# Performance work log

Measured on AMD Instinct MI355X. Metric: run time of the kernel, lower is better.

Reference implementation:

```python
import jax, jax.numpy as jnp
import numpy as np

K = 60
BATCH, NCLS, H, W = 8, 2, 512, 512


def _neighbors(x):
    # x: [B,H,W] int32 in {0,1}. Returns P2..P9 clockwise starting north.
    p = jnp.pad(x, ((0, 0), (1, 1), (1, 1)))
    P2 = p[:, :-2, 1:-1]   # N
    P3 = p[:, :-2, 2:]     # NE
    P4 = p[:, 1:-1, 2:]    # E
    P5 = p[:, 2:, 2:]      # SE
    P6 = p[:, 2:, 1:-1]    # S
    P7 = p[:, 2:, :-2]     # SW
    P8 = p[:, 1:-1, :-2]   # W
    P9 = p[:, :-2, :-2]    # NW
    return P2, P3, P4, P5, P6, P7, P8, P9


def _substep(x, first):
    # One Zhang-Suen thinning sub-iteration (the algorithm used by
    # skimage.morphology.skeletonize for 2D images).
    P2, P3, P4, P5, P6, P7, P8, P9 = _neighbors(x)
    seq = (P2, P3, P4, P5, P6, P7, P8, P9, P2)
    # A = number of 0->1 transitions in circular neighbor sequence
    A = sum(((seq[i] == 0) & (seq[i + 1] == 1)).astype(jnp.int32) for i in range(8))
    Bn = P2 + P3 + P4 + P5 + P6 + P7 + P8 + P9
    if first:
        c3 = P2 * P4 * P6
        c4 = P4 * P6 * P8
    else:
        c3 = P2 * P4 * P8
        c4 = P2 * P6 * P8
    delete = (x == 1) & (Bn >= 2) & (Bn <= 6) & (A == 1) & (c3 == 0) & (c4 == 0)
    return x * (1 - delete.astype(x.dtype))


def _skeletonize(img):
    # img: [B,H,W] int32 binary. Iterate thinning until fixed point.
    def body(state):
        x, _ = state
        x2 = _substep(_substep(x, True), False)
        return x2, jnp.any(x2 != x)

    def cond(state):
        return state[1]

    out, _ = jax.lax.while_loop(cond, body, (img, jnp.array(True)))
    return out


def _conv(x, kernel, pad):
    # x: [B,1,H,W], kernel: [1,1,k,k], 'same' padding pad
    return jax.lax.conv_general_dilated(x, kernel, (1, 1), [(pad, pad), (pad, pad)])


def setup_inputs() -> dict:
    key = jax.random.key(0)
    k1, k2 = jax.random.split(key)
    pred = jax.random.normal(k1, (BATCH, NCLS, H, W), dtype=jnp.float32)
    target = jax.random.randint(k2, (BATCH, H, W), 0, NCLS, dtype=jnp.int32)
    return {"pred": pred, "target": target}


def reference(pred, target):
    # Per-pixel cross entropy, reduction='none'
    logp = jax.nn.log_softmax(pred, axis=1)
    L = -jnp.take_along_axis(logp, target[:, None].astype(jnp.int32), axis=1)[:, 0]  # [B,H,W]

    # Skeletonize the hard prediction (nonzero = foreground)
    A = jnp.argmax(pred, axis=1)
    skel = _skeletonize((A != 0).astype(jnp.int32))  # [B,H,W]
    Bm = skel[:, None].astype(pred.dtype)            # [B,1,H,W]

    # 3x3 neighbor count (center zeroed); endpoints C where product == 1
    k3 = jnp.ones((1, 1, 3, 3), pred.dtype).at[0, 0, 1, 1].set(0.0)
    C = Bm * _conv(Bm, k3, 1)
    C = (C == 1.0).astype(pred.dtype)

    # 9x9 endpoint density, scaled by K; zeros -> weight 1
    k9 = jnp.ones((1, 1, 9, 9), pred.dtype)
    N = _conv(C, k9, 4) * K
    Wmap = N + (N == 0.0).astype(pred.dtype)  # [B,1,H,W]

    return jnp.mean(Wmap[:, 0] * L)
```

## Files before the change

### kernel.cpp

```cpp
#include <hip/hip_runtime.h>

#define BATCH   8
#define HH      512
#define WW      512
#define IMGPIX  (HH * WW)
#define NPIX    (BATCH * IMGPIX)
#define NWORDS  (NPIX / 64)
#define WPR     8
#define LDSTR   9
#define FPSCALE 262144.0
#define MAXPAIR 256

typedef unsigned long long u64;
typedef unsigned int u32;

__global__ void prep_kernel(const float* __restrict__ pred, const int* __restrict__ target,
                            float* __restrict__ L, u64* __restrict__ xp,
                            u64* __restrict__ acc64, u32* __restrict__ ticket) {
    int i = blockIdx.x * blockDim.x + threadIdx.x;
    if (i == 0) { acc64[0] = 0ULL; ticket[0] = 0u; }
    if (i >= NPIX) return;
    int b = i >> 18;
    int hw = i & (IMGPIX - 1);
    float p0 = pred[((size_t)(2 * b) << 18) + hw];
    float p1 = pred[((size_t)(2 * b + 1) << 18) + hw];
    float m = fmaxf(p0, p1);
    float lse = m + logf(expf(p0 - m) + expf(p1 - m));
    int t = target[i];
    L[i] = lse - (t ? p1 : p0);
    u64 word = __ballot(p1 > p0);
    if ((threadIdx.x & 63) == 0) xp[i >> 6] = word;
}

#define FA(a,b,c,s,cy) { u64 _x = (a)^(b); (s) = _x^(c); (cy) = ((a)&(b)) | ((c)&_x); }
#define HA(a,b,s,cy)   { (s) = (a)^(b); (cy) = (a)&(b); }

template<int FIRST>
__device__ __forceinline__ u64 zs_row(const u64* __restrict__ U, u64* __restrict__ M,
                                      const u64* __restrict__ D)
{
    u64 ch = 0;
    #pragma unroll
    for (int k = 0; k < WPR; ++k) {
        u64 Mc = M[k];
        if (Mc == 0ULL) continue;
        u64 Uc = U[k], Dc = D[k];
        u64 Up = k     ? U[k-1] : 0ULL;
        u64 Mp = k     ? M[k-1] : 0ULL;
        u64 Dp = k     ? D[k-1] : 0ULL;
        u64 Un = k < 7 ? U[k+1] : 0ULL;
        u64 Mn = k < 7 ? M[k+1] : 0ULL;
        u64 Dn = k < 7 ? D[k+1] : 0ULL;
        u64 P2 = Uc, P6 = Dc;
        u64 P3 = (Uc >> 1) | (Un << 63);
        u64 P4 = (Mc >> 1) | (Mn << 63);
        u64 P5 = (Dc >> 1) | (Dn << 63);
        u64 P9 = (Uc << 1) | (Up >> 63);
        u64 P8 = (Mc << 1) | (Mp >> 63);
        u64 P7 = (Dc << 1) | (Dp >> 63);

        u64 sa,ca, sb,cb, sc,cc, b0,cd, sd,ce, b1,cf, b2,b3;
        FA(P2,P3,P4, sa,ca);
        FA(P5,P6,P7, sb,cb);
        FA(P8,P9,sa, sc,cc);
        HA(sb,sc,    b0,cd);
        FA(ca,cb,cc, sd,ce);
        HA(sd,cd,    b1,cf);
        HA(ce,cf,    b2,b3);
        u64 ge2 = b1 | b2 | b3;
        u64 le6 = ~(b3 | (b0 & b1 & b2));

        u64 e, seen, two = 0;
        seen = (~P2) & P3;
        e = (~P3) & P4; two |= seen & e; seen |= e;
        e = (~P4) & P5; two |= seen & e; seen |= e;
        e = (~P5) & P6; two |= seen & e; seen |= e;
        e = (~P6) & P7; two |= seen & e; seen |= e;
        e = (~P7) & P8; two |= seen & e; seen |= e;
        e = (~P8) & P9; two |= seen & e; seen |= e;
        e = (~P9) & P2; two |= seen & e; seen |= e;
        u64 A1 = seen & ~two;

        u64 c34;
        if (FIRST) { u64 t = P4 & P6; c34 = t & (P2 | P8); }
        else       { u64 t = P2 & P8; c34 = t & (P4 | P6); }

        u64 del = Mc & ge2 & le6 & A1 & ~c34;
        M[k] = Mc ^ del;
        ch |= del;
    }
    return ch;
}

__global__ __launch_bounds__(512)
void skel_kernel(const u64* __restrict__ xp, u64* __restrict__ eg)
{
    __shared__ u64 img[(HH + 2) * LDSTR];
    const int b = blockIdx.x;
    const int h = threadIdx.x;
    const int base = (h + 1) * LDSTR;

    if (h < 2 * LDSTR) {
        int idx = (h < LDSTR) ? h : ((HH + 1) * LDSTR + (h - LDSTR));
        img[idx] = 0ULL;
    }

    u64 M[WPR], U[WPR], D[WPR];
    const u64* src = xp + ((size_t)b << 12) + (size_t)h * WPR;
    #pragma unroll
    for (int k = 0; k < WPR; ++k) { M[k] = src[k]; img[base + k] = M[k]; }
    __syncthreads();

    for (int p = 0; p < MAXPAIR; ++p) {
        #pragma unroll
        for (int k = 0; k < WPR; ++k) { U[k] = img[base - LDSTR + k]; D[k] = img[base + LDSTR + k]; }
        __syncthreads();
        u64 chA = zs_row<1>(U, M, D);
        if (chA) {
            #pragma unroll
            for (int k = 0; k < WPR; ++k) img[base + k] = M[k];
        }
        __syncthreads();

        #pragma unroll
        for (int k = 0; k < WPR; ++k) { U[k] = img[base - LDSTR + k]; D[k] = img[base + LDSTR + k]; }
        __syncthreads();
        u64 chB = zs_row<0>(U, M, D);
        if (chB) {
            #pragma unroll
            for (int k = 0; k < WPR; ++k) img[base + k] = M[k];
        }
        if (!__syncthreads_or((chA | chB) != 0ULL)) break;
    }

    #pragma unroll
    for (int k = 0; k < WPR; ++k) { U[k] = img[base - LDSTR + k]; D[k] = img[base + LDSTR + k]; }
    u64* egr = eg + ((size_t)b << 12) + (size_t)h * WPR;
    #pragma unroll
    for (int k = 0; k < WPR; ++k) {
        u64 Mc = M[k];
        u64 Uc = U[k], Dc = D[k];
        u64 Up = k     ? U[k-1] : 0ULL;
        u64 Mp = k     ? M[k-1] : 0ULL;
        u64 Dp = k     ? D[k-1] : 0ULL;
        u64 Un = k < 7 ? U[k+1] : 0ULL;
        u64 Mn = k < 7 ? M[k+1] : 0ULL;
        u64 Dn = k < 7 ? D[k+1] : 0ULL;
        u64 P2 = Uc, P6 = Dc;
        u64 P3 = (Uc >> 1) | (Un << 63);
        u64 P4 = (Mc >> 1) | (Mn << 63);
        u64 P5 = (Dc >> 1) | (Dn << 63);
        u64 P9 = (Uc << 1) | (Up >> 63);
        u64 P8 = (Mc << 1) | (Mp >> 63);
        u64 P7 = (Dc << 1) | (Dp >> 63);
        u64 e, seen, two = 0;
        seen = P2;
        e = P3; two |= seen & e; seen |= e;
        e = P4; two |= seen & e; seen |= e;
        e = P5; two |= seen & e; seen |= e;
        e = P6; two |= seen & e; seen |= e;
        e = P7; two |= seen & e; seen |= e;
        e = P8; two |= seen & e; seen |= e;
        e = P9; two |= seen & e; seen |= e;
        egr[k] = Mc & seen & ~two;
    }
}

struct Planes { u64 p0, p1, p2, p3; };

__device__ __forceinline__ Planes vcount9(const u64 r[9]) {
    u64 s0,c0, s1,c1, s2,c2, p0,t0, t1,t2, p1,t3, p2,p3;
    FA(r[0],r[1],r[2], s0,c0);
    FA(r[3],r[4],r[5], s1,c1);
    FA(r[6],r[7],r[8], s2,c2);
    FA(s0,s1,s2, p0,t0);
    FA(c0,c1,c2, t1,t2);
    HA(t0,t1,    p1,t3);
    HA(t2,t3,    p2,p3);
    Planes P; P.p0 = p0; P.p1 = p1; P.p2 = p2; P.p3 = p3; return P;
}

__device__ __forceinline__ u64 spread8(u64 bb) {
    u64 s = (bb * 0x0101010101010101ULL) & 0x8040201008040201ULL;
    return ((s + 0x7f7f7f7f7f7f7f7fULL) >> 7) & 0x0101010101010101ULL;
}

__device__ __forceinline__ u64 vbytes(const Planes& P, int g) {
    int s = 8 * g;
    return  spread8((P.p0 >> s) & 0xFFULL)
         + (spread8((P.p1 >> s) & 0xFFULL) << 1)
         + (spread8((P.p2 >> s) & 0xFFULL) << 2)
         + (spread8((P.p3 >> s) & 0xFFULL) << 3);
}

__global__ __launch_bounds__(256)
void final_kernel(const float* __restrict__ L, const u64* __restrict__ eg,
                  u64* __restrict__ acc64, u32* __restrict__ ticket,
                  float* __restrict__ out) {
    __shared__ float sm[256];
    int wi = blockIdx.x * blockDim.x + threadIdx.x;
    int b  = wi >> 12;
    int h  = (wi >> 3) & (HH - 1);
    int wc = wi & 7;
    const u64* img = eg + ((size_t)b << 12);

    u64 rows[3][9];
    #pragma unroll
    for (int dh = -4; dh <= 4; ++dh) {
        int hh = h + dh;
        bool okh = (unsigned)hh < (unsigned)HH;
        const u64* rp = img + hh * WPR;
        rows[0][dh + 4] = (okh && wc > 0) ? rp[wc - 1] : 0ULL;
        rows[1][dh + 4] = okh             ? rp[wc]     : 0ULL;
        rows[2][dh + 4] = (okh && wc < 7) ? rp[wc + 1] : 0ULL;
    }
    Planes Pm = vcount9(rows[0]);
    Planes Pc = vcount9(rows[1]);
    Planes Pp = vcount9(rows[2]);

    u64 v[10];
    v[0] = vbytes(Pm, 7);
    #pragma unroll
    for (int g = 0; g < 8; ++g) v[g + 1] = vbytes(Pc, g);
    v[9] = vbytes(Pp, 0);

    const float4* Lr = (const float4*)(L + ((size_t)wi << 6));
    float acc = 0.0f;
    #pragma unroll
    for (int g = 0; g < 8; ++g) {
        u64 a = v[g + 1], lo = v[g], hi = v[g + 2];
        u64 n = a;
        #pragma unroll
        for (int d = 1; d <= 4; ++d) {
            n += (a >> (8 * d)) | (hi << (64 - 8 * d));
            n += (a << (8 * d)) | (lo >> (64 - 8 * d));
        }
        float4 f0 = Lr[2 * g], f1 = Lr[2 * g + 1];
        #pragma unroll
        for (int j = 0; j < 8; ++j) {
            int cnt = (int)((n >> (8 * j)) & 0xFFULL);
            float wgt = cnt ? (float)(60 * cnt) : 1.0f;
            float lv = (j < 4) ? ((j == 0) ? f0.x : (j == 1) ? f0.y : (j == 2) ? f0.z : f0.w)
                               : ((j == 4) ? f1.x : (j == 5) ? f1.y : (j == 6) ? f1.z : f1.w);
            acc += wgt * lv;
        }
    }

    sm[threadIdx.x] = acc;
    __syncthreads();
    for (int s = 128; s > 0; s >>= 1) {
        if (threadIdx.x < s) sm[threadIdx.x] += sm[threadIdx.x + s];
        __syncthreads();
    }
    if (threadIdx.x == 0) {
        u64 vfx = (u64)(long long)llrintf(sm[0] * (float)FPSCALE);
        atomicAdd(acc64, vfx);
        __threadfence();
        u32 t = atomicAdd(ticket, 1u);
        if (t == (u32)(gridDim.x - 1)) {
            __threadfence();
            u64 total = __hip_atomic_load(acc64, __ATOMIC_RELAXED, __HIP_MEMORY_SCOPE_AGENT);
            out[0] = (float)((double)(long long)total / (FPSCALE * (double)NPIX));
        }
    }
}

extern "C" void kernel_launch(void* const* d_in, const int* in_sizes, int n_in,
                              void* d_out, int out_size, void* d_ws, size_t ws_size,
                              hipStream_t stream) {
    const float* pred = (const float*)d_in[0];
    const int* target = (const int*)d_in[1];
    float* out = (float*)d_out;
    char* ws = (char*)d_ws;

    float* L    = (float*)(ws);
    u64* xp     = (u64*)(ws + 8388608);
    u64* eg     = (u64*)(ws + 8650752);
    u64* acc64  = (u64*)(ws + 8912896);
    u32* ticket = (u32*)(ws + 8912904);

    prep_kernel<<<dim3(NPIX / 256), dim3(256), 0, stream>>>(pred, target, L, xp, acc64, ticket);
    skel_kernel<<<dim3(BATCH), dim3(512), 0, stream>>>(xp, eg);
    final_kernel<<<dim3(NWORDS / 256), dim3(256), 0, stream>>>(L, eg, acc64, ticket, out);
}
```

Before: 61.77 us.

## Double-buffer skeleton LDS to halve barriers and swizzle row layout

Replaces the single padded shared image with two ping-pong buffers, so each sub-iteration writes into the other buffer and the barrier after the neighbour reads is no longer needed. That cuts four barriers per pass to two. Rows now use an XOR swizzle instead of a stride-9 pad to avoid bank conflicts, and boundary rows become predicated zeros instead of padding rows. Rows are always written back, not only when changed, and the prep kernel's log-sum-exp now uses fast __expf/__logf intrinsics, which slightly reduces precision.

```diff
diff --git a/kernel.cpp b/kernel.cpp
--- a/kernel.cpp
+++ b/kernel.cpp
@@ -7,7 +7,6 @@
 #define NPIX    (BATCH * IMGPIX)
 #define NWORDS  (NPIX / 64)
 #define WPR     8
-#define LDSTR   9
 #define FPSCALE 262144.0
 #define MAXPAIR 256
 
@@ -24,8 +23,8 @@
     int hw = i & (IMGPIX - 1);
     float p0 = pred[((size_t)(2 * b) << 18) + hw];
     float p1 = pred[((size_t)(2 * b + 1) << 18) + hw];
-    float m = fmaxf(p0, p1);
-    float lse = m + logf(expf(p0 - m) + expf(p1 - m));
+    float ad = fabsf(p0 - p1);
+    float lse = fmaxf(p0, p1) + __logf(1.0f + __expf(-ad));
     int t = target[i];
     L[i] = lse - (t ? p1 : p0);
     u64 word = __ballot(p1 > p0);
@@ -92,49 +91,52 @@
     return ch;
 }
 
+__device__ __forceinline__ int sidx(int h, int k) {
+    return (h << 3) + (k ^ ((h >> 1) & 7));
+}
+
 __global__ __launch_bounds__(512)
 void skel_kernel(const u64* __restrict__ xp, u64* __restrict__ eg)
 {
-    __shared__ u64 img[(HH + 2) * LDSTR];
+    __shared__ u64 buf[2][HH * WPR];
     const int b = blockIdx.x;
     const int h = threadIdx.x;
-    const int base = (h + 1) * LDSTR;
-
-    if (h < 2 * LDSTR) {
-        int idx = (h < LDSTR) ? h : ((HH + 1) * LDSTR + (h - LDSTR));
-        img[idx] = 0ULL;
-    }
 
     u64 M[WPR], U[WPR], D[WPR];
     const u64* src = xp + ((size_t)b << 12) + (size_t)h * WPR;
     #pragma unroll
-    for (int k = 0; k < WPR; ++k) { M[k] = src[k]; img[base + k] = M[k]; }
+    for (int k = 0; k < WPR; ++k) { M[k] = src[k]; buf[0][sidx(h, k)] = M[k]; }
     __syncthreads();
 
+    const bool hasU = (h > 0), hasD = (h < HH - 1);
+
     for (int p = 0; p < MAXPAIR; ++p) {
         #pragma unroll
-        for (int k = 0; k < WPR; ++k) { U[k] = img[base - LDSTR + k]; D[k] = img[base + LDSTR + k]; }
+        for (int k = 0; k < WPR; ++k) {
+            U[k] = hasU ? buf[0][sidx(h - 1, k)] : 0ULL;
+            D[k] = hasD ? buf[0][sidx(h + 1, k)] : 0ULL;
+        }
+        u64 chA = zs_row<1>(U, M, D);
+        #pragma unroll
+        for (int k = 0; k < WPR; ++k) buf[1][sidx(h, k)] = M[k];
         __syncthreads();
-        u64 chA = zs_row<1>(U, M, D);
-        if (chA) {
-            #pragma unroll
-            for (int k = 0; k < WPR; ++k) img[base + k] = M[k];
-        }
-        __syncthreads();
-
-        #pragma unroll
-        for (int k = 0; k < WPR; ++k) { U[k] = img[base - LDSTR + k]; D[k] = img[base + LDSTR + k]; }
-        __syncthreads();
+
+        #pragma unroll
+        for (int k = 0; k < WPR; ++k) {
+            U[k] = hasU ? buf[1][sidx(h - 1, k)] : 0ULL;
+            D[k] = hasD ? buf[1][sidx(h + 1, k)] : 0ULL;
+        }
         u64 chB = zs_row<0>(U, M, D);
-        if (chB) {
-            #pragma unroll
-            for (int k = 0; k < WPR; ++k) img[base + k] = M[k];
-        }
+        #pragma unroll
+        for (int k = 0; k < WPR; ++k) buf[0][sidx(h, k)] = M[k];
         if (!__syncthreads_or((chA | chB) != 0ULL)) break;
     }
 
     #pragma unroll
-    for (int k = 0; k < WPR; ++k) { U[k] = img[base - LDSTR + k]; D[k] = img[base + LDSTR + k]; }
+    for (int k = 0; k < WPR; ++k) {
+        U[k] = hasU ? buf[0][sidx(h - 1, k)] : 0ULL;
+        D[k] = hasD ? buf[0][sidx(h + 1, k)] : 0ULL;
+    }
     u64* egr = eg + ((size_t)b << 12) + (size_t)h * WPR;
     #pragma unroll
     for (int k = 0; k < WPR; ++k) {
```

New measurement: 59.45 us. 1.04x faster.
